# Optimization experiments

Measured on AMD Instinct MI355X. Metric: run time of the kernel, lower is better.

## Reference

```python
import jax, jax.numpy as jnp
import numpy as np

N = 50000
LN_EPS = 1e-5
NEG_SLOPE = 0.2


def layer_norm(x, w, b):
    mu = jnp.mean(x, axis=-1, keepdims=True)
    var = jnp.mean((x - mu) ** 2, axis=-1, keepdims=True)
    return (x - mu) * jax.lax.rsqrt(var + LN_EPS) * w + b


def gat_conv(x, src, dst, W, a_src, a_dst, bias, concat):
    # W: [in, H*D]; a_src/a_dst: [H, D]
    H, D = a_src.shape
    h = (x @ W).reshape(-1, H, D)                      # [N, H, D]
    s = jnp.einsum('nhd,hd->nh', h, a_src)             # alpha contribution of source
    t = jnp.einsum('nhd,hd->nh', h, a_dst)             # alpha contribution of target
    e = jax.nn.leaky_relu(s[src] + t[dst], NEG_SLOPE)  # [E, H] edge logits
    m = jax.ops.segment_max(e, dst, num_segments=N)    # segment softmax over incoming edges
    p = jnp.exp(e - m[dst])
    z = jax.ops.segment_sum(p, dst, num_segments=N)
    alpha = p / (z[dst] + 1e-16)                       # [E, H]
    out = jax.ops.segment_sum(alpha[:, :, None] * h[src], dst, num_segments=N)  # [N, H, D]
    out = out.reshape(N, H * D) if concat else out.mean(axis=1)
    return out + bias


def setup_inputs() -> dict:
    key = jax.random.key(0)
    ks = jax.random.split(key, 16)
    IN, HID, OUT, H1, H2 = 256, 32, 40, 6, 3
    E = 800000
    g = lambda k, shp, fan: jax.random.normal(k, shp, jnp.float32) * (1.0 / np.sqrt(fan))
    inp = {
        'x': jax.random.normal(ks[0], (N, IN), jnp.float32),
        'edge_index': jax.random.randint(ks[1], (2, E), 0, N, jnp.int32),
        'W1': g(ks[2], (IN, H1 * HID), IN), 'a1s': g(ks[3], (H1, HID), HID), 'a1d': g(ks[4], (H1, HID), HID),
        'b1': jnp.zeros((H1 * HID,), jnp.float32),
        'ln1w': jnp.ones((H1 * HID,), jnp.float32), 'ln1b': jnp.zeros((H1 * HID,), jnp.float32),
        'W2': g(ks[5], (H1 * HID, H2 * HID), H1 * HID), 'a2s': g(ks[6], (H2, HID), HID), 'a2d': g(ks[7], (H2, HID), HID),
        'b2': jnp.zeros((H2 * HID,), jnp.float32),
        'ln2w': jnp.ones((H2 * HID,), jnp.float32), 'ln2b': jnp.zeros((H2 * HID,), jnp.float32),
        'W3': g(ks[8], (H2 * HID, 1 * OUT), H2 * HID), 'a3s': g(ks[9], (1, OUT), OUT), 'a3d': g(ks[10], (1, OUT), OUT),
        'b3': jnp.zeros((OUT,), jnp.float32),
        'ln3w': jnp.ones((OUT,), jnp.float32), 'ln3b': jnp.zeros((OUT,), jnp.float32),
    }
    return inp


def reference(x, edge_index, W1, a1s, a1d, b1, ln1w, ln1b,
              W2, a2s, a2d, b2, ln2w, ln2b,
              W3, a3s, a3d, b3, ln3w, ln3b):
    # add self-loops (PyG GATConv default); eval mode -> dropouts are identity
    loop = jnp.arange(N, dtype=edge_index.dtype)
    src = jnp.concatenate([edge_index[0], loop])
    dst = jnp.concatenate([edge_index[1], loop])

    h = gat_conv(x, src, dst, W1, a1s, a1d, b1, concat=True)
    h = jax.nn.elu(layer_norm(h, ln1w, ln1b))
    h = gat_conv(h, src, dst, W2, a2s, a2d, b2, concat=True)
    h = jax.nn.elu(layer_norm(h, ln2w, ln2b))
    h = gat_conv(h, src, dst, W3, a3s, a3d, b3, concat=False)
    h = layer_norm(h, ln3w, ln3b)
    return jax.nn.log_softmax(h, axis=1)
```

## Files before the change

kernel.cpp:

```cpp
#include <hip/hip_runtime.h>
#include <hip/hip_bf16.h>
#include <cstdint>

#define NNODES 50000
#define NEDGES 800000
#define ETOT   (NEDGES + NNODES)
#define LN_EPS 1e-5f
#define NEG_SLOPE 0.2f
#define ELLW   64

typedef __attribute__((ext_vector_type(8))) short s16x8;
typedef __attribute__((ext_vector_type(4))) float f32x4;

__device__ __forceinline__ float bf2f(unsigned short u) {
    return __uint_as_float(((unsigned int)u) << 16);
}
__device__ __forceinline__ unsigned short f2bf(float f) {
    unsigned int u = __float_as_uint(f);
    u += 0x7FFFu + ((u >> 16) & 1u);
    return (unsigned short)(u >> 16);
}
__device__ __forceinline__ float plo32(unsigned u) { return __uint_as_float(u << 16); }
__device__ __forceinline__ float phi32(unsigned u) { return __uint_as_float(u & 0xffff0000u); }


#define W1SZ (192 * 256)
#define W2SZ (96 * 192)
#define W3SZ (48 * 96)

__global__ __launch_bounds__(256) void prep_kernel(const float* __restrict__ W1, const float* __restrict__ W2,
                                                   const float* __restrict__ W3, unsigned short* __restrict__ wt1,
                                                   unsigned short* __restrict__ wt2, unsigned short* __restrict__ wt3,
                                                   int* __restrict__ counts, int* __restrict__ ell) {
    int i = blockIdx.x * 256 + threadIdx.x;
    if (i < NNODES) {
        counts[i] = 1;
        ell[i * ELLW] = i;
    }
    if (i < W1SZ) {
        int c = i >> 8, k = i & 255;
        int n = c >> 4, r = c & 15;
        wt1[((n * 32 + (k >> 3)) * 16 + r) * 8 + (k & 7)] = f2bf(W1[k * 192 + c]);
    } else if (i < W1SZ + W2SZ) {
        int j = i - W1SZ;
        int c = j / 192, k = j - c * 192;
        int n = c >> 4, r = c & 15;
        wt2[((n * 24 + (k >> 3)) * 16 + r) * 8 + (k & 7)] = f2bf(W2[k * 96 + c]);
    } else if (i < W1SZ + W2SZ + W3SZ) {
        int j = i - (W1SZ + W2SZ);
        int c = j / 96, k = j - c * 96;
        int n = c >> 4, r = c & 15;
        wt3[((n * 12 + (k >> 3)) * 16 + r) * 8 + (k & 7)] = (c < 40) ? f2bf(W3[k * 40 + c]) : (unsigned short)0;
    }
}


template<int K, int F, int CS, int FP, int H, int D, int SPAD, int WSPLIT, int NHW, bool ABF, bool FILL>
__global__ __launch_bounds__(256, 4) void gemmst_kernel(const void* __restrict__ Xv,
                                                        const unsigned short* __restrict__ Wt,
                                                        unsigned short* __restrict__ C,
                                                        const float* __restrict__ asf, const float* __restrict__ adf,
                                                        float* __restrict__ sbuf, float* __restrict__ tbuf,
                                                        int nrows, int gblocks,
                                                        const int* __restrict__ eidx, int* counts,
                                                        int* __restrict__ ell, int e) {
    if constexpr (FILL) {
        if (blockIdx.x >= (unsigned)gblocks) {
            int i = ((int)blockIdx.x - gblocks) * 256 + (int)threadIdx.x;
            if (i < e) {
                int sv = eidx[i];
                int d  = eidx[e + i];
                int slot = atomicAdd(&counts[d], 1);
                if (slot < ELLW) ell[d * ELLW + slot] = sv;
            }
            return;
        }
    }
    constexpr int NT  = FP / 16;
    constexpr int NTW = NT / WSPLIT;
    constexpr int TPB = 4 / WSPLIT;

    __shared__ float lds_s[TPB][16][H];
    __shared__ float lds_t[TPB][16][H];

    const int w    = threadIdx.x >> 6;
    const int lane = threadIdx.x & 63;
    const int tile = w / WSPLIT;
    const int sub  = w % WSPLIT;
    const int pb   = sub * NTW;
    const int mbase = ((int)blockIdx.x * TPB + tile) * 16;
    const int r = lane & 15;
    const int q = lane >> 4;

    if constexpr (WSPLIT == 1) {
        if (mbase >= nrows) return;
    }

    f32x4 acc[NTW];
#pragma unroll
    for (int nn = 0; nn < NTW; ++nn) acc[nn] = (f32x4){0.f, 0.f, 0.f, 0.f};

    int arow = mbase + r;
    if (arow >= nrows) arow = nrows - 1;
    if (arow < 0) arow = 0;
    const unsigned short* xb = (const unsigned short*)Xv + (size_t)arow * K;
    const float* xf = (const float*)Xv + (size_t)arow * K;

#pragma unroll 2
    for (int k0 = 0; k0 < K; k0 += 32) {
        const int kk = k0 + q * 8;
        const unsigned kc = (unsigned)(kk >> 3);
        s16x8 a;
        if constexpr (ABF) {
            a = *reinterpret_cast<const s16x8*>(xb + kk);
        } else {
            float4 lo = *reinterpret_cast<const float4*>(xf + kk);
            float4 hi = *reinterpret_cast<const float4*>(xf + kk + 4);
            a[0] = (short)f2bf(lo.x); a[1] = (short)f2bf(lo.y);
            a[2] = (short)f2bf(lo.z); a[3] = (short)f2bf(lo.w);
            a[4] = (short)f2bf(hi.x); a[5] = (short)f2bf(hi.y);
            a[6] = (short)f2bf(hi.z); a[7] = (short)f2bf(hi.w);
        }
#pragma unroll
        for (int nn = 0; nn < NTW; ++nn) {
            const unsigned gn = (unsigned)(pb + nn);
            s16x8 b = *reinterpret_cast<const s16x8*>(Wt + ((gn * (K / 8) + kc) * 16 + (unsigned)r) * 8);
            acc[nn] = __builtin_amdgcn_mfma_f32_16x16x32_bf16(a, b, acc[nn], 0, 0, 0);
        }
    }

#pragma unroll
    for (int nn = 0; nn < NTW; ++nn) {
        int col = (pb + nn) * 16 + r;
        if (col < F) {
#pragma unroll
            for (int i = 0; i < 4; ++i) {
                int row = mbase + q * 4 + i;
                if (row < nrows) C[(size_t)row * CS + col] = f2bf(acc[nn][i]);
            }
        }
    }

    float ps[4][NHW], pt[4][NHW];
#pragma unroll
    for (int i = 0; i < 4; ++i)
#pragma unroll
        for (int lh = 0; lh < NHW; ++lh) { ps[i][lh] = 0.f; pt[i][lh] = 0.f; }
    const int h_lo = (sub * NTW * 16) / D;
#pragma unroll
    for (int ss = 0; ss < WSPLIT; ++ss) {
        if (ss != sub) continue;
#pragma unroll
        for (int nn = 0; nn < NTW; ++nn) {
            const int gn = ss * NTW + nn;
            const int col = gn * 16 + r;
            const int lh = (gn * 16) / D - (ss * NTW * 16) / D;
            float av = (col < F) ? asf[col] : 0.f;
            float dv = (col < F) ? adf[col] : 0.f;
#pragma unroll
            for (int i = 0; i < 4; ++i) {
                ps[i][lh] = fmaf(acc[nn][i], av, ps[i][lh]);
                pt[i][lh] = fmaf(acc[nn][i], dv, pt[i][lh]);
            }
        }
    }
#pragma unroll
    for (int off = 1; off <= 8; off <<= 1) {
#pragma unroll
        for (int i = 0; i < 4; ++i)
#pragma unroll
            for (int lh = 0; lh < NHW; ++lh) {
                ps[i][lh] += __shfl_xor(ps[i][lh], off);
                pt[i][lh] += __shfl_xor(pt[i][lh], off);
            }
    }

    if constexpr (WSPLIT == 1) {
#pragma unroll
        for (int lh = 0; lh < NHW; ++lh) {
            const int gh = lh;
            if (gh < H && r == gh) {
#pragma unroll
                for (int i = 0; i < 4; ++i) {
                    int row = mbase + q * 4 + i;
                    if (row < nrows) {
                        sbuf[row * SPAD + gh] = ps[i][lh];
                        tbuf[row * H + gh]    = pt[i][lh];
                    }
                }
            }
        }
    } else {
        constexpr int NE = TPB * 16 * H;
        if ((int)threadIdx.x < NE) {
            int idx = threadIdx.x;
            int t2 = idx / (16 * H), rem = idx % (16 * H);
            lds_s[t2][rem / H][rem % H] = 0.f;
            lds_t[t2][rem / H][rem % H] = 0.f;
        }
        __syncthreads();
#pragma unroll
        for (int lh = 0; lh < NHW; ++lh) {
            const int gh = h_lo + lh;
            if (gh < H && r == gh) {
#pragma unroll
                for (int i = 0; i < 4; ++i) {
                    atomicAdd(&lds_s[tile][q * 4 + i][gh], ps[i][lh]);
                    atomicAdd(&lds_t[tile][q * 4 + i][gh], pt[i][lh]);
                }
            }
        }
        __syncthreads();
        if ((int)threadIdx.x < NE) {
            int idx = threadIdx.x;
            int t2 = idx / (16 * H), rem = idx % (16 * H);
            int rw = rem / H, hh = rem % H;
            int row = (int)blockIdx.x * TPB * 16 + t2 * 16 + rw;
            if (row < nrows) {
                sbuf[row * SPAD + hh] = lds_s[t2][rw][hh];
                tbuf[row * H + hh]    = lds_t[t2][rw][hh];
            }
        }
    }
}


template<int H, int D, int FS, int CPL, int SPAD, int MODE, typename OutT>
__global__ __launch_bounds__(256) void agg7_kernel(const unsigned short* __restrict__ feat,
                                                   const float* __restrict__ sb, const float* __restrict__ tb,
                                                   const int* __restrict__ counts, const int* __restrict__ ell,
                                                   const float* __restrict__ bias, const float* __restrict__ lnw,
                                                   const float* __restrict__ lnb, OutT* __restrict__ out, int n) {
    constexpr int F = H * D;
    constexpr int NL = F / CPL;
    int wid = (blockIdx.x * blockDim.x + threadIdx.x) >> 6;
    int lane = threadIdx.x & 63;
    if (wid >= n) return;
    const int node = wid;
    const int base = node * ELLW;
    int cnt = counts[node];
    if (cnt > ELLW) cnt = ELLW;
    const bool act = lane < NL;
    const unsigned ch0 = (unsigned)(lane < NL ? lane : 0) * CPL;
    const int h = (int)(ch0 / D);
    const float th = tb[node * H + h];

    float z = 0.f;
    float acc[CPL];
#pragma unroll
    for (int c = 0; c < CPL; ++c) acc[c] = 0.f;

    auto pval = [&](float sv) -> float {
        float e = sv + th;
        e = fmaxf(e, NEG_SLOPE * e);
        return __expf(e);
    };
    auto fmae = [&](float p, const unsigned short* fp) {
        if constexpr (CPL == 4) {
            uint2 w = *reinterpret_cast<const uint2*>(fp);
            acc[0] = fmaf(p, plo32(w.x), acc[0]);
            acc[1] = fmaf(p, phi32(w.x), acc[1]);
            acc[2] = fmaf(p, plo32(w.y), acc[2]);
            acc[3] = fmaf(p, phi32(w.y), acc[3]);
        } else if constexpr (CPL == 2) {
            unsigned w = *reinterpret_cast<const unsigned*>(fp);
            acc[0] = fmaf(p, plo32(w), acc[0]);
            acc[1] = fmaf(p, phi32(w), acc[1]);
        } else {
            acc[0] = fmaf(p, bf2f(*fp), acc[0]);
        }
    };

    int j = 0;
    for (; j + 7 < cnt; j += 8) {
        int4 snA = *reinterpret_cast<const int4*>(ell + base + j);
        int4 snB = *reinterpret_cast<const int4*>(ell + base + j + 4);
        unsigned o0 = (unsigned)snA.x * FS + ch0;
        unsigned o1 = (unsigned)snA.y * FS + ch0;
        unsigned o2 = (unsigned)snA.z * FS + ch0;
        unsigned o3 = (unsigned)snA.w * FS + ch0;
        unsigned o4 = (unsigned)snB.x * FS + ch0;
        unsigned o5 = (unsigned)snB.y * FS + ch0;
        unsigned o6 = (unsigned)snB.z * FS + ch0;
        unsigned o7 = (unsigned)snB.w * FS + ch0;
        if (act) {
            float s0 = sb[(unsigned)snA.x * SPAD + h];
            float s1 = sb[(unsigned)snA.y * SPAD + h];
            float s2 = sb[(unsigned)snA.z * SPAD + h];
            float s3 = sb[(unsigned)snA.w * SPAD + h];
            float s4 = sb[(unsigned)snB.x * SPAD + h];
            float s5 = sb[(unsigned)snB.y * SPAD + h];
            float s6 = sb[(unsigned)snB.z * SPAD + h];
            float s7 = sb[(unsigned)snB.w * SPAD + h];
            if constexpr (CPL == 4) {
                uint2 w0 = *reinterpret_cast<const uint2*>(feat + o0);
                uint2 w1 = *reinterpret_cast<const uint2*>(feat + o1);
                uint2 w2 = *reinterpret_cast<const uint2*>(feat + o2);
                uint2 w3 = *reinterpret_cast<const uint2*>(feat + o3);
                uint2 w4 = *reinterpret_cast<const uint2*>(feat + o4);
                uint2 w5 = *reinterpret_cast<const uint2*>(feat + o5);
                uint2 w6 = *reinterpret_cast<const uint2*>(feat + o6);
                uint2 w7 = *reinterpret_cast<const uint2*>(feat + o7);
                float p0 = pval(s0), p1 = pval(s1), p2 = pval(s2), p3 = pval(s3);
                float p4 = pval(s4), p5 = pval(s5), p6 = pval(s6), p7 = pval(s7);
                z += ((p0 + p1) + (p2 + p3)) + ((p4 + p5) + (p6 + p7));
                acc[0] = fmaf(p0, plo32(w0.x), acc[0]); acc[1] = fmaf(p0, phi32(w0.x), acc[1]);
                acc[2] = fmaf(p0, plo32(w0.y), acc[2]); acc[3] = fmaf(p0, phi32(w0.y), acc[3]);
                acc[0] = fmaf(p1, plo32(w1.x), acc[0]); acc[1] = fmaf(p1, phi32(w1.x), acc[1]);
                acc[2] = fmaf(p1, plo32(w1.y), acc[2]); acc[3] = fmaf(p1, phi32(w1.y), acc[3]);
                acc[0] = fmaf(p2, plo32(w2.x), acc[0]); acc[1] = fmaf(p2, phi32(w2.x), acc[1]);
                acc[2] = fmaf(p2, plo32(w2.y), acc[2]); acc[3] = fmaf(p2, phi32(w2.y), acc[3]);
                acc[0] = fmaf(p3, plo32(w3.x), acc[0]); acc[1] = fmaf(p3, phi32(w3.x), acc[1]);
                acc[2] = fmaf(p3, plo32(w3.y), acc[2]); acc[3] = fmaf(p3, phi32(w3.y), acc[3]);
                acc[0] = fmaf(p4, plo32(w4.x), acc[0]); acc[1] = fmaf(p4, phi32(w4.x), acc[1]);
                acc[2] = fmaf(p4, plo32(w4.y), acc[2]); acc[3] = fmaf(p4, phi32(w4.y), acc[3]);
                acc[0] = fmaf(p5, plo32(w5.x), acc[0]); acc[1] = fmaf(p5, phi32(w5.x), acc[1]);
                acc[2] = fmaf(p5, plo32(w5.y), acc[2]); acc[3] = fmaf(p5, phi32(w5.y), acc[3]);
                acc[0] = fmaf(p6, plo32(w6.x), acc[0]); acc[1] = fmaf(p6, phi32(w6.x), acc[1]);
                acc[2] = fmaf(p6, plo32(w6.y), acc[2]); acc[3] = fmaf(p6, phi32(w6.y), acc[3]);
                acc[0] = fmaf(p7, plo32(w7.x), acc[0]); acc[1] = fmaf(p7, phi32(w7.x), acc[1]);
                acc[2] = fmaf(p7, plo32(w7.y), acc[2]); acc[3] = fmaf(p7, phi32(w7.y), acc[3]);
            } else if constexpr (CPL == 2) {
                unsigned w0 = *reinterpret_cast<const unsigned*>(feat + o0);
                unsigned w1 = *reinterpret_cast<const unsigned*>(feat + o1);
                unsigned w2 = *reinterpret_cast<const unsigned*>(feat + o2);
                unsigned w3 = *reinterpret_cast<const unsigned*>(feat + o3);
                unsigned w4 = *reinterpret_cast<const unsigned*>(feat + o4);
                unsigned w5 = *reinterpret_cast<const unsigned*>(feat + o5);
                unsigned w6 = *reinterpret_cast<const unsigned*>(feat + o6);
                unsigned w7 = *reinterpret_cast<const unsigned*>(feat + o7);
                float p0 = pval(s0), p1 = pval(s1), p2 = pval(s2), p3 = pval(s3);
                float p4 = pval(s4), p5 = pval(s5), p6 = pval(s6), p7 = pval(s7);
                z += ((p0 + p1) + (p2 + p3)) + ((p4 + p5) + (p6 + p7));
                acc[0] = fmaf(p0, plo32(w0), acc[0]); acc[1] = fmaf(p0, phi32(w0), acc[1]);
                acc[0] = fmaf(p1, plo32(w1), acc[0]); acc[1] = fmaf(p1, phi32(w1), acc[1]);
                acc[0] = fmaf(p2, plo32(w2), acc[0]); acc[1] = fmaf(p2, phi32(w2), acc[1]);
                acc[0] = fmaf(p3, plo32(w3), acc[0]); acc[1] = fmaf(p3, phi32(w3), acc[1]);
                acc[0] = fmaf(p4, plo32(w4), acc[0]); acc[1] = fmaf(p4, phi32(w4), acc[1]);
                acc[0] = fmaf(p5, plo32(w5), acc[0]); acc[1] = fmaf(p5, phi32(w5), acc[1]);
                acc[0] = fmaf(p6, plo32(w6), acc[0]); acc[1] = fmaf(p6, phi32(w6), acc[1]);
                acc[0] = fmaf(p7, plo32(w7), acc[0]); acc[1] = fmaf(p7, phi32(w7), acc[1]);
            } else {
                unsigned short w0 = feat[o0], w1 = feat[o1], w2 = feat[o2], w3 = feat[o3];
                unsigned short w4 = feat[o4], w5 = feat[o5], w6 = feat[o6], w7 = feat[o7];
                float p0 = pval(s0), p1 = pval(s1), p2 = pval(s2), p3 = pval(s3);
                float p4 = pval(s4), p5 = pval(s5), p6 = pval(s6), p7 = pval(s7);
                z += ((p0 + p1) + (p2 + p3)) + ((p4 + p5) + (p6 + p7));
                acc[0] = fmaf(p0, bf2f(w0), acc[0]);
                acc[0] = fmaf(p1, bf2f(w1), acc[0]);
                acc[0] = fmaf(p2, bf2f(w2), acc[0]);
                acc[0] = fmaf(p3, bf2f(w3), acc[0]);
                acc[0] = fmaf(p4, bf2f(w4), acc[0]);
                acc[0] = fmaf(p5, bf2f(w5), acc[0]);
                acc[0] = fmaf(p6, bf2f(w6), acc[0]);
                acc[0] = fmaf(p7, bf2f(w7), acc[0]);
            }
        }
    }
    for (; j + 3 < cnt; j += 4) {
        int4 snA = *reinterpret_cast<const int4*>(ell + base + j);
        if (act) {
            float p0 = pval(sb[(unsigned)snA.x * SPAD + h]);
            float p1 = pval(sb[(unsigned)snA.y * SPAD + h]);
            float p2 = pval(sb[(unsigned)snA.z * SPAD + h]);
            float p3 = pval(sb[(unsigned)snA.w * SPAD + h]);
            z += (p0 + p1) + (p2 + p3);
            fmae(p0, feat + (unsigned)snA.x * FS + ch0);
            fmae(p1, feat + (unsigned)snA.y * FS + ch0);
            fmae(p2, feat + (unsigned)snA.z * FS + ch0);
            fmae(p3, feat + (unsigned)snA.w * FS + ch0);
        }
    }
    for (; j < cnt; ++j) {
        int sn = ell[base + j];
        if (act) {
            float p = pval(sb[(unsigned)sn * SPAD + h]);
            z += p;
            fmae(p, feat + (unsigned)sn * FS + ch0);
        }
    }

    const float zinv = 1.f / (z + 1e-16f);
    float v[CPL];
    float sum = 0.f, sumsq = 0.f;
#pragma unroll
    for (int c = 0; c < CPL; ++c) v[c] = 0.f;
    if (act) {
#pragma unroll
        for (int c = 0; c < CPL; ++c) {
            v[c] = fmaf(acc[c], zinv, bias[ch0 + c]);
            sum += v[c];
            sumsq += v[c] * v[c];
        }
    }
#pragma unroll
    for (int off = 32; off; off >>= 1) {
        sum += __shfl_xor(sum, off);
        sumsq += __shfl_xor(sumsq, off);
    }
    const float mu = sum / F;
    const float var = sumsq / F - mu * mu;
    const float rstd = rsqrtf(var + LN_EPS);

    if (MODE == 0) {
        if (act) {
            unsigned short yb[CPL];
#pragma unroll
            for (int c = 0; c < CPL; ++c) {
                float y = (v[c] - mu) * rstd * lnw[ch0 + c] + lnb[ch0 + c];
                y = y > 0.f ? y : expm1f(y);
                yb[c] = f2bf(y);
            }
            OutT* op = out + (size_t)node * F + ch0;
            if constexpr (CPL == 4) {
                ushort4 st = {yb[0], yb[1], yb[2], yb[3]};
                *reinterpret_cast<ushort4*>(op) = st;
            } else if constexpr (CPL == 2) {
                ushort2 st = {yb[0], yb[1]};
                *reinterpret_cast<ushort2*>(op) = st;
            } else {
                *op = yb[0];
            }
        }
    } else {
        float y = 0.f, mx = -1e30f;
        if (act) {
            y = (v[0] - mu) * rstd * lnw[ch0] + lnb[ch0];
            mx = y;
        }
#pragma unroll
        for (int off = 32; off; off >>= 1) mx = fmaxf(mx, __shfl_xor(mx, off));
        float se = act ? __expf(y - mx) : 0.f;
#pragma unroll
        for (int off = 32; off; off >>= 1) se += __shfl_xor(se, off);
        float lse = logf(se);
        if (act) ((float*)out)[(size_t)node * F + ch0] = y - mx - lse;
    }
}


static inline size_t align_up(size_t x) { return (x + 255) & ~(size_t)255; }

extern "C" void kernel_launch(void* const* d_in, const int* in_sizes, int n_in,
                              void* d_out, int out_size, void* d_ws, size_t ws_size,
                              hipStream_t stream) {
    const float* x    = (const float*)d_in[0];
    const int*   eidx = (const int*)d_in[1];
    const float* W1   = (const float*)d_in[2];
    const float* a1s  = (const float*)d_in[3];
    const float* a1d  = (const float*)d_in[4];
    const float* b1   = (const float*)d_in[5];
    const float* ln1w = (const float*)d_in[6];
    const float* ln1b = (const float*)d_in[7];
    const float* W2   = (const float*)d_in[8];
    const float* a2s  = (const float*)d_in[9];
    const float* a2d  = (const float*)d_in[10];
    const float* b2   = (const float*)d_in[11];
    const float* ln2w = (const float*)d_in[12];
    const float* ln2b = (const float*)d_in[13];
    const float* W3   = (const float*)d_in[14];
    const float* a3s  = (const float*)d_in[15];
    const float* a3d  = (const float*)d_in[16];
    const float* b3   = (const float*)d_in[17];
    const float* ln3w = (const float*)d_in[18];
    const float* ln3b = (const float*)d_in[19];

    char* w = (char*)d_ws;
    int* counts = (int*)w;  w += align_up((size_t)NNODES * 4);
    int* ell    = (int*)w;  w += align_up((size_t)NNODES * ELLW * 4);
    unsigned short* bufA = (unsigned short*)w; w += align_up((size_t)NNODES * 192 * 2);
    unsigned short* bufB = (unsigned short*)w; w += align_up((size_t)NNODES * 192 * 2);
    float* sbuf = (float*)w; w += align_up((size_t)NNODES * 8 * 4);
    float* tbuf = (float*)w; w += align_up((size_t)NNODES * 8 * 4);
    unsigned short* wt1 = (unsigned short*)w; w += align_up((size_t)W1SZ * 2);
    unsigned short* wt2 = (unsigned short*)w; w += align_up((size_t)W2SZ * 2);
    unsigned short* wt3 = (unsigned short*)w; w += align_up((size_t)W3SZ * 2);

    const int BS = 256;
    const int PREP_N = W1SZ + W2SZ + W3SZ;
    prep_kernel<<<(PREP_N + BS - 1) / BS, BS, 0, stream>>>(W1, W2, W3, wt1, wt2, wt3, counts, ell);

    const int G1 = NNODES / 16;
    const int G2 = (NNODES + 31) / 32;
    const int G3 = (NNODES + 63) / 64;
    const int FILL_NB  = (NEDGES + BS - 1) / BS;
    const int GRID_AGG = (NNODES + 3) / 4;

    gemmst_kernel<256, 192, 192, 192, 6, 32, 8, 4, 2, false, true>
        <<<G1 + FILL_NB, BS, 0, stream>>>(x, wt1, bufA, a1s, a1d, sbuf, tbuf, NNODES,
                                          G1, eidx, counts, ell, NEDGES);
    agg7_kernel<6, 32, 192, 4, 8, 0, unsigned short><<<GRID_AGG, BS, 0, stream>>>(bufA, sbuf, tbuf, counts, ell, b1, ln1w, ln1b, bufB, NNODES);

    gemmst_kernel<192, 96, 128, 96, 3, 32, 4, 2, 2, true, false>
        <<<G2, BS, 0, stream>>>(bufB, wt2, bufA, a2s, a2d, sbuf, tbuf, NNODES,
                                G2, nullptr, nullptr, nullptr, 0);
    agg7_kernel<3, 32, 128, 2, 4, 0, unsigned short><<<GRID_AGG, BS, 0, stream>>>(bufA, sbuf, tbuf, counts, ell, b2, ln2w, ln2b, bufB, NNODES);

    gemmst_kernel<96, 40, 64, 48, 1, 40, 1, 1, 1, true, false>
        <<<G3, BS, 0, stream>>>(bufB, wt3, bufA, a3s, a3d, sbuf, tbuf, NNODES,
                                G3, nullptr, nullptr, nullptr, 0);
    agg7_kernel<1, 40, 64, 1, 1, 1, float><<<GRID_AGG, BS, 0, stream>>>(bufA, sbuf, tbuf, counts, ell, b3, ln3w, ln3b, (float*)d_out, NNODES);
}
```

Before: 266.7 us.

## Store ELL neighbor indices as 16-bit and put edge-fill blocks first

Changes the ELL adjacency array from int32 to uint16 indices, which halves the index storage and the bytes each aggregation read of the neighbor list costs. The aggregation kernels now unpack 8 indices from one 16-byte load. In the fused GEMM kernel the edge-fill blocks are also moved to the front of the grid so the atomic scatter gets scheduled before the GEMM tiles. Node ids go up to 49999, so they fit in 16 bits, but the code no longer works if the node count exceeds 65535.

```diff
diff --git a/kernel.cpp b/kernel.cpp
--- a/kernel.cpp
+++ b/kernel.cpp
@@ -31,11 +31,11 @@
 __global__ __launch_bounds__(256) void prep_kernel(const float* __restrict__ W1, const float* __restrict__ W2,
                                                    const float* __restrict__ W3, unsigned short* __restrict__ wt1,
                                                    unsigned short* __restrict__ wt2, unsigned short* __restrict__ wt3,
-                                                   int* __restrict__ counts, int* __restrict__ ell) {
+                                                   int* __restrict__ counts, unsigned short* __restrict__ ell) {
     int i = blockIdx.x * 256 + threadIdx.x;
     if (i < NNODES) {
         counts[i] = 1;
-        ell[i * ELLW] = i;
+        ell[(size_t)i * ELLW] = (unsigned short)i;
     }
     if (i < W1SZ) {
         int c = i >> 8, k = i & 255;
@@ -61,21 +61,23 @@
                                                         unsigned short* __restrict__ C,
                                                         const float* __restrict__ asf, const float* __restrict__ adf,
                                                         float* __restrict__ sbuf, float* __restrict__ tbuf,
-                                                        int nrows, int gblocks,
+                                                        int nrows, int fillnb,
                                                         const int* __restrict__ eidx, int* counts,
-                                                        int* __restrict__ ell, int e) {
+                                                        unsigned short* __restrict__ ell, int e) {
     if constexpr (FILL) {
-        if (blockIdx.x >= (unsigned)gblocks) {
-            int i = ((int)blockIdx.x - gblocks) * 256 + (int)threadIdx.x;
+        if (blockIdx.x < (unsigned)fillnb) {
+            int i = (int)blockIdx.x * 256 + (int)threadIdx.x;
             if (i < e) {
                 int sv = eidx[i];
                 int d  = eidx[e + i];
                 int slot = atomicAdd(&counts[d], 1);
-                if (slot < ELLW) ell[d * ELLW + slot] = sv;
+                if (slot < ELLW) ell[(size_t)d * ELLW + slot] = (unsigned short)sv;
             }
             return;
         }
     }
+    const int bix = FILL ? ((int)blockIdx.x - fillnb) : (int)blockIdx.x;
+
     constexpr int NT  = FP / 16;
     constexpr int NTW = NT / WSPLIT;
     constexpr int TPB = 4 / WSPLIT;
@@ -88,7 +90,7 @@
     const int tile = w / WSPLIT;
     const int sub  = w % WSPLIT;
     const int pb   = sub * NTW;
-    const int mbase = ((int)blockIdx.x * TPB + tile) * 16;
+    const int mbase = (bix * TPB + tile) * 16;
     const int r = lane & 15;
     const int q = lane >> 4;
 
@@ -215,7 +217,7 @@
             int idx = threadIdx.x;
             int t2 = idx / (16 * H), rem = idx % (16 * H);
             int rw = rem / H, hh = rem % H;
-            int row = (int)blockIdx.x * TPB * 16 + t2 * 16 + rw;
+            int row = bix * TPB * 16 + t2 * 16 + rw;
             if (row < nrows) {
                 sbuf[row * SPAD + hh] = lds_s[t2][rw][hh];
                 tbuf[row * H + hh]    = lds_t[t2][rw][hh];
@@ -226,9 +228,9 @@
 
 
 template<int H, int D, int FS, int CPL, int SPAD, int MODE, typename OutT>
-__global__ __launch_bounds__(256) void agg7_kernel(const unsigned short* __restrict__ feat,
+__global__ __launch_bounds__(256) void agg8_kernel(const unsigned short* __restrict__ feat,
                                                    const float* __restrict__ sb, const float* __restrict__ tb,
-                                                   const int* __restrict__ counts, const int* __restrict__ ell,
+                                                   const int* __restrict__ counts, const unsigned short* __restrict__ ell,
                                                    const float* __restrict__ bias, const float* __restrict__ lnw,
                                                    const float* __restrict__ lnb, OutT* __restrict__ out, int n) {
     constexpr int F = H * D;
@@ -237,7 +239,7 @@
     int lane = threadIdx.x & 63;
     if (wid >= n) return;
     const int node = wid;
-    const int base = node * ELLW;
+    const unsigned short* __restrict__ ellp = ell + (size_t)node * ELLW;
     int cnt = counts[node];
     if (cnt > ELLW) cnt = ELLW;
     const bool act = lane < NL;
@@ -273,25 +275,22 @@
 
     int j = 0;
     for (; j + 7 < cnt; j += 8) {
-        int4 snA = *reinterpret_cast<const int4*>(ell + base + j);
-        int4 snB = *reinterpret_cast<const int4*>(ell + base + j + 4);
-        unsigned o0 = (unsigned)snA.x * FS + ch0;
-        unsigned o1 = (unsigned)snA.y * FS + ch0;
-        unsigned o2 = (unsigned)snA.z * FS + ch0;
-        unsigned o3 = (unsigned)snA.w * FS + ch0;
-        unsigned o4 = (unsigned)snB.x * FS + ch0;
-        unsigned o5 = (unsigned)snB.y * FS + ch0;
-        unsigned o6 = (unsigned)snB.z * FS + ch0;
-        unsigned o7 = (unsigned)snB.w * FS + ch0;
+        uint4 iv = *reinterpret_cast<const uint4*>(ellp + j);
+        unsigned i0 = iv.x & 0xffffu, i1 = iv.x >> 16;
+        unsigned i2 = iv.y & 0xffffu, i3 = iv.y >> 16;
+        unsigned i4 = iv.z & 0xffffu, i5 = iv.z >> 16;
+        unsigned i6 = iv.w & 0xffffu, i7 = iv.w >> 16;
+        unsigned o0 = i0 * FS + ch0, o1 = i1 * FS + ch0, o2 = i2 * FS + ch0, o3 = i3 * FS + ch0;
+        unsigned o4 = i4 * FS + ch0, o5 = i5 * FS + ch0, o6 = i6 * FS + ch0, o7 = i7 * FS + ch0;
         if (act) {
-            float s0 = sb[(unsigned)snA.x * SPAD + h];
-            float s1 = sb[(unsigned)snA.y * SPAD + h];
-            float s2 = sb[(unsigned)snA.z * SPAD + h];
-            float s3 = sb[(unsigned)snA.w * SPAD + h];
-            float s4 = sb[(unsigned)snB.x * SPAD + h];
-            float s5 = sb[(unsigned)snB.y * SPAD + h];
-            float s6 = sb[(unsigned)snB.z * SPAD + h];
-            float s7 = sb[(unsigned)snB.w * SPAD + h];
+            float s0 = sb[i0 * SPAD + h];
+            float s1 = sb[i1 * SPAD + h];
+            float s2 = sb[i2 * SPAD + h];
+            float s3 = sb[i3 * SPAD + h];
+            float s4 = sb[i4 * SPAD + h];
+            float s5 = sb[i5 * SPAD + h];
+            float s6 = sb[i6 * SPAD + h];
+            float s7 = sb[i7 * SPAD + h];
             if constexpr (CPL == 4) {
                 uint2 w0 = *reinterpret_cast<const uint2*>(feat + o0);
                 uint2 w1 = *reinterpret_cast<const uint2*>(feat + o1);
@@ -358,25 +357,27 @@
         }
     }
     for (; j + 3 < cnt; j += 4) {
-        int4 snA = *reinterpret_cast<const int4*>(ell + base + j);
+        uint2 iv = *reinterpret_cast<const uint2*>(ellp + j);
+        unsigned i0 = iv.x & 0xffffu, i1 = iv.x >> 16;
+        unsigned i2 = iv.y & 0xffffu, i3 = iv.y >> 16;
         if (act) {
-            float p0 = pval(sb[(unsigned)snA.x * SPAD + h]);
-            float p1 = pval(sb[(unsigned)snA.y * SPAD + h]);
-            float p2 = pval(sb[(unsigned)snA.z * SPAD + h]);
-            float p3 = pval(sb[(unsigned)snA.w * SPAD + h]);
+            float p0 = pval(sb[i0 * SPAD + h]);
+            float p1 = pval(sb[i1 * SPAD + h]);
+            float p2 = pval(sb[i2 * SPAD + h]);
+            float p3 = pval(sb[i3 * SPAD + h]);
             z += (p0 + p1) + (p2 + p3);
-            fmae(p0, feat + (unsigned)snA.x * FS + ch0);
-            fmae(p1, feat + (unsigned)snA.y * FS + ch0);
-            fmae(p2, feat + (unsigned)snA.z * FS + ch0);
-            fmae(p3, feat + (unsigned)snA.w * FS + ch0);
+            fmae(p0, feat + i0 * FS + ch0);
+            fmae(p1, feat + i1 * FS + ch0);
+            fmae(p2, feat + i2 * FS + ch0);
+            fmae(p3, feat + i3 * FS + ch0);
         }
     }
     for (; j < cnt; ++j) {
-        int sn = ell[base + j];
+        unsigned sn = ellp[j];
         if (act) {
-            float p = pval(sb[(unsigned)sn * SPAD + h]);
+            float p = pval(sb[sn * SPAD + h]);
             z += p;
-            fmae(p, feat + (unsigned)sn * FS + ch0);
+            fmae(p, feat + sn * FS + ch0);
         }
     }
 
@@ -467,7 +468,7 @@
 
     char* w = (char*)d_ws;
     int* counts = (int*)w;  w += align_up((size_t)NNODES * 4);
-    int* ell    = (int*)w;  w += align_up((size_t)NNODES * ELLW * 4);
+    unsigned short* ell = (unsigned short*)w;  w += align_up((size_t)NNODES * ELLW * 2);
     unsigned short* bufA = (unsigned short*)w; w += align_up((size_t)NNODES * 192 * 2);
     unsigned short* bufB = (unsigned short*)w; w += align_up((size_t)NNODES * 192 * 2);
     float* sbuf = (float*)w; w += align_up((size_t)NNODES * 8 * 4);
@@ -487,17 +488,17 @@
     const int GRID_AGG = (NNODES + 3) / 4;
 
     gemmst_kernel<256, 192, 192, 192, 6, 32, 8, 4, 2, false, true>
-        <<<G1 + FILL_NB, BS, 0, stream>>>(x, wt1, bufA, a1s, a1d, sbuf, tbuf, NNODES,
-                                          G1, eidx, counts, ell, NEDGES);
-    agg7_kernel<6, 32, 192, 4, 8, 0, unsigned short><<<GRID_AGG, BS, 0, stream>>>(bufA, sbuf, tbuf, counts, ell, b1, ln1w, ln1b, bufB, NNODES);
+        <<<FILL_NB + G1, BS, 0, stream>>>(x, wt1, bufA, a1s, a1d, sbuf, tbuf, NNODES,
+                                          FILL_NB, eidx, counts, ell, NEDGES);
+    agg8_kernel<6, 32, 192, 4, 8, 0, unsigned short><<<GRID_AGG, BS, 0, stream>>>(bufA, sbuf, tbuf, counts, ell, b1, ln1w, ln1b, bufB, NNODES);
 
     gemmst_kernel<192, 96, 128, 96, 3, 32, 4, 2, 2, true, false>
         <<<G2, BS, 0, stream>>>(bufB, wt2, bufA, a2s, a2d, sbuf, tbuf, NNODES,
-                                G2, nullptr, nullptr, nullptr, 0);
-    agg7_kernel<3, 32, 128, 2, 4, 0, unsigned short><<<GRID_AGG, BS, 0, stream>>>(bufA, sbuf, tbuf, counts, ell, b2, ln2w, ln2b, bufB, NNODES);
+                                0, nullptr, nullptr, nullptr, 0);
+    agg8_kernel<3, 32, 128, 2, 4, 0, unsigned short><<<GRID_AGG, BS, 0, stream>>>(bufA, sbuf, tbuf, counts, ell, b2, ln2w, ln2b, bufB, NNODES);
 
     gemmst_kernel<96, 40, 64, 48, 1, 40, 1, 1, 1, true, false>
         <<<G3, BS, 0, stream>>>(bufB, wt3, bufA, a3s, a3d, sbuf, tbuf, NNODES,
-                                G3, nullptr, nullptr, nullptr, 0);
-    agg7_kernel<1, 40, 64, 1, 1, 1, float><<<GRID_AGG, BS, 0, stream>>>(bufA, sbuf, tbuf, counts, ell, b3, ln3w, ln3b, (float*)d_out, NNODES);
+                                0, nullptr, nullptr, nullptr, 0);
+    agg8_kernel<1, 40, 64, 1, 1, 1, float><<<GRID_AGG, BS, 0, stream>>>(bufA, sbuf, tbuf, counts, ell, b3, ln3w, ln3b, (float*)d_out, NNODES);
 }
```

Result: no change. 264.8 us (-0.7%).
